# Performance work log

Measured on AMD Instinct MI355X. Metric: run time of the kernel, lower is better.

The kernel has to match this reference:

```python
import jax, jax.numpy as jnp
import numpy as np

NUM_HEADS = 16
PREFIX_LEN = 256


def setup_inputs() -> dict:
    key = jax.random.key(0)
    k1, k2, k3, k4 = jax.random.split(key, 4)
    bs, seq_len, dim = 2, 2048, 1024
    x = jax.random.normal(k1, (bs, seq_len, dim), dtype=jnp.float32)
    # torch Linear weights: (out_features, in_features)
    qkv_w = jax.random.normal(k2, (3 * dim, dim), dtype=jnp.float32) * (dim ** -0.5)
    proj_w = jax.random.normal(k3, (dim, dim), dtype=jnp.float32) * (dim ** -0.5)
    proj_b = jax.random.normal(k4, (dim,), dtype=jnp.float32) * 0.01
    # prefix tokens (visible to everyone): first PREFIX_LEN positions
    prefix_mask = (jnp.arange(seq_len)[None, :] < PREFIX_LEN) & jnp.ones((bs, 1), bool)
    return {"x": x, "qkv_w": qkv_w, "proj_w": proj_w, "proj_b": proj_b,
            "prefix_mask": prefix_mask, "num_patches": 2048}


def reference(x, qkv_w, proj_w, proj_b, prefix_mask, num_patches):
    bs, seq_len, dim = x.shape
    h, hd = NUM_HEADS, dim // NUM_HEADS

    # fused QKV projection (no bias)
    qkv = x @ qkv_w.T                                  # (bs, S, 3*dim)
    q, k, v = jnp.split(qkv, 3, axis=-1)
    q = q.reshape(bs, seq_len, h, hd).transpose(0, 2, 1, 3)  # (bs, h, S, hd)
    k = k.reshape(bs, seq_len, h, hd).transpose(0, 2, 1, 3)
    v = v.reshape(bs, seq_len, h, hd).transpose(0, 2, 1, 3)

    # prefix-causal mask: causal tril OR prefix columns, sliced to (S, S)
    tril = jnp.tril(jnp.ones((num_patches, num_patches), dtype=bool))[:seq_len, :seq_len]
    mask = jnp.logical_or(tril[None, :, :], prefix_mask[:, None, :])  # (bs, S, S)

    scores = jnp.einsum('bhqd,bhkd->bhqk', q, k) / jnp.sqrt(jnp.float32(hd))
    scores = jnp.where(mask[:, None, :, :], scores, -jnp.inf)
    attn = jax.nn.softmax(scores, axis=-1)
    out = jnp.einsum('bhqk,bhkd->bhqd', attn, v)       # (bs, h, S, hd)
    out = out.transpose(0, 2, 1, 3).reshape(bs, seq_len, dim)
    return out @ proj_w.T + proj_b
```

## Files before the change

kernel.cpp:

```cpp
#include <hip/hip_runtime.h>
#include <cstdint>

typedef __attribute__((ext_vector_type(8))) _Float16 half8;
typedef __attribute__((ext_vector_type(4))) _Float16 half4;
typedef __attribute__((ext_vector_type(2))) __fp16 fp16x2;
typedef __attribute__((ext_vector_type(4))) float f32x4;

union H8 { half8 v; unsigned u[4]; };
union H2U { fp16x2 h; unsigned u; };

__device__ __forceinline__ void gld_lds16(const void* g, void* l) {
  __builtin_amdgcn_global_load_lds(
      (const __attribute__((address_space(1))) unsigned int*)g,
      (__attribute__((address_space(3))) unsigned int*)l, 16, 0, 0);
}

__global__ __launch_bounds__(256) void cast3_kernel(
    const float* __restrict__ x, const float* __restrict__ w1,
    const float* __restrict__ w2, _Float16* __restrict__ out) {
  int i = blockIdx.x * 256 + threadIdx.x;
  const float* src;
  int off;
  if (i < 1048576)      { src = x;  off = i; }
  else if (i < 1835008) { src = w1; off = i - 1048576; }
  else                  { src = w2; off = i - 1835008; }
  float4 v = ((const float4*)src)[off];
  half4 h;
  h[0] = (_Float16)v.x; h[1] = (_Float16)v.y;
  h[2] = (_Float16)v.z; h[3] = (_Float16)v.w;
  ((half4*)out)[i] = h;
}

template <int EPI>
__global__ __launch_bounds__(256) void gemm_bt(
    const _Float16* __restrict__ A, const _Float16* __restrict__ B, int K,
    _Float16* __restrict__ Qb, _Float16* __restrict__ Kb, _Float16* __restrict__ VbT,
    float* __restrict__ Out, const float* __restrict__ Bias) {
  __shared__ _Float16 Asm[128 * 64];
  __shared__ _Float16 Bsm[128 * 64];
  const int tid = threadIdx.x;
  const int wave = tid >> 6, lane = tid & 63;
  const int l16 = lane & 15, lg = lane >> 4;
  const int m0 = blockIdx.y * 128, n0 = blockIdx.x * 128;
  const int wr = wave >> 1, wc = wave & 1;
  f32x4 acc[4][4] = {};

  int srow[4], sofs[4];
#pragma unroll
  for (int i = 0; i < 4; i++) {
    int c = tid + i * 256;
    srow[i] = c >> 3;
    sofs[i] = ((c & 7) ^ (srow[i] & 7)) * 8;
  }
  const int rb0 = ((lg) ^ (l16 & 7)) * 16;
  const int rb1 = ((4 + lg) ^ (l16 & 7)) * 16;

  for (int k0 = 0; k0 < K; k0 += 64) {
    __syncthreads();
#pragma unroll
    for (int i = 0; i < 4; i++) {
      int c = tid + i * 256;
      gld_lds16(A + (size_t)(m0 + srow[i]) * K + k0 + sofs[i], (char*)Asm + c * 16);
      gld_lds16(B + (size_t)(n0 + srow[i]) * K + k0 + sofs[i], (char*)Bsm + c * 16);
    }
    __syncthreads();
#pragma unroll
    for (int kc = 0; kc < 2; kc++) {
      const int rb = kc ? rb1 : rb0;
      half8 af[4], bf[4];
#pragma unroll
      for (int f = 0; f < 4; f++) {
        af[f] = *(const half8*)((char*)Asm + (wr * 64 + f * 16 + l16) * 128 + rb);
        bf[f] = *(const half8*)((char*)Bsm + (wc * 64 + f * 16 + l16) * 128 + rb);
      }
#pragma unroll
      for (int i = 0; i < 4; i++)
#pragma unroll
        for (int j = 0; j < 4; j++)
          acc[i][j] = __builtin_amdgcn_mfma_f32_16x16x32_f16(af[i], bf[j], acc[i][j], 0, 0, 0);
    }
  }

  if (EPI == 0) {
#pragma unroll
    for (int i = 0; i < 4; i++) {
      int mbase = m0 + wr * 64 + i * 16 + lg * 4;
      int b = mbase >> 11, s = mbase & 2047;
#pragma unroll
      for (int j = 0; j < 4; j++) {
        int n = n0 + wc * 64 + j * 16 + l16;
        int part = n >> 10, f = n & 1023;
        int h = f >> 6, d = f & 63;
        if (part == 2) {
          int x = s & 31;
          int sp = (s & ~31) | (((x >> 2) & 3) << 3) | (((x >> 4) & 1) << 2);
          half4 v;
          v[0] = (_Float16)acc[i][j][0]; v[1] = (_Float16)acc[i][j][1];
          v[2] = (_Float16)acc[i][j][2]; v[3] = (_Float16)acc[i][j][3];
          *(half4*)(VbT + (((size_t)b * 16 + h) * 64 + d) * 2048 + sp) = v;
        } else {
          _Float16* dst = (part == 0) ? Qb : Kb;
          float scale = (part == 0) ? 0.125f : 1.0f;
#pragma unroll
          for (int r = 0; r < 4; r++)
            dst[(((size_t)b * 16 + h) * 2048 + (s + r)) * 64 + d] =
                (_Float16)(acc[i][j][r] * scale);
        }
      }
    }
  } else {
#pragma unroll
    for (int i = 0; i < 4; i++) {
      int mbase = m0 + wr * 64 + i * 16 + lg * 4;
#pragma unroll
      for (int j = 0; j < 4; j++) {
        int n = n0 + wc * 64 + j * 16 + l16;
        float bias = Bias[n];
#pragma unroll
        for (int r = 0; r < 4; r++) {
          int m = mbase + r;
          Out[(size_t)m * 1024 + n] = acc[i][j][r] + bias;
        }
      }
    }
  }
}

__global__ __launch_bounds__(256) void attn_kernel(
    const _Float16* __restrict__ Qb, const _Float16* __restrict__ Kb,
    const _Float16* __restrict__ VbT, _Float16* __restrict__ AO) {
  __shared__ _Float16 Ks[2][64 * 64];
  __shared__ _Float16 Vt[2][64 * 64];
  const int bh = blockIdx.x;
  const int q0 = (31 - blockIdx.y) * 64;
  const int tid = threadIdx.x, wave = tid >> 6, lane = tid & 63;
  const int l16 = lane & 15, lg = lane >> 4;
  const int qw = q0 + wave * 16;
  const size_t bhbase = (size_t)bh * 2048 * 64;
  const _Float16* Kbb = Kb + bhbase;
  const _Float16* Vbb = VbT + bhbase;

  const int c0 = tid, c1 = tid + 256;
  const int kofs0 = ((c0 >> 3) * 64) + (((c0 & 7) ^ ((c0 >> 3) & 7)) * 8);
  const int kofs1 = ((c1 >> 3) * 64) + (((c1 & 7) ^ ((c1 >> 3) & 7)) * 8);
  const int vofs0 = ((c0 >> 3) * 2048) + (((c0 & 7) ^ ((c0 >> 3) & 7)) * 8);
  const int vofs1 = ((c1 >> 3) * 2048) + (((c1 & 7) ^ ((c1 >> 3) & 7)) * 8);

  half8 qf[2];
#pragma unroll
  for (int kc = 0; kc < 2; kc++)
    qf[kc] = *(const half8*)(Qb + bhbase + (size_t)(qw + l16) * 64 + kc * 32 + lg * 8);

  f32x4 oacc[4] = {};
  float mrun = -1e30f, lrun = 0.f;
  const int kend = (q0 + 64 > 256) ? (q0 + 64) : 256;

  const int xv = (l16 & 7) << 4;
  const int rb0 = l16 * 128 + ((lg * 16) ^ xv);
  const int rb1 = l16 * 128 + ((64 + lg * 16) ^ xv);

  auto STAGE = [&](int buf, int j0) {
    gld_lds16(Kbb + j0 * 64 + kofs0, (char*)Ks[buf] + c0 * 16);
    gld_lds16(Kbb + j0 * 64 + kofs1, (char*)Ks[buf] + c1 * 16);
    gld_lds16(Vbb + j0 + vofs0, (char*)Vt[buf] + c0 * 16);
    gld_lds16(Vbb + j0 + vofs1, (char*)Vt[buf] + c1 * 16);
  };

  STAGE(0, 0);
  int cur = 0;
  for (int j0 = 0; j0 < kend; j0 += 64) {
    __syncthreads();
    if (j0 + 64 < kend) STAGE(cur ^ 1, j0 + 64);
    const char* Kc = (const char*)Ks[cur];
    const char* Vc = (const char*)Vt[cur];

    f32x4 sf[4] = {};
#pragma unroll
    for (int kc = 0; kc < 2; kc++) {
      const int rb = kc ? rb1 : rb0;
#pragma unroll
      for (int jb = 0; jb < 4; jb++) {
        half8 kf = *(const half8*)(Kc + jb * 2048 + rb);
        sf[jb] = __builtin_amdgcn_mfma_f32_16x16x32_f16(kf, qf[kc], sf[jb], 0, 0, 0);
      }
    }

    if (j0 + 63 >= 256 && j0 + 63 > qw) {
      const int stok = qw + l16;
#pragma unroll
      for (int jb = 0; jb < 4; jb++)
#pragma unroll
        for (int r = 0; r < 4; r++) {
          int j = j0 + jb * 16 + lg * 4 + r;
          if (j > stok && j >= 256) sf[jb][r] = -1e30f;
        }
    }

    float a0 = fmaxf(fmaxf(sf[0][0], sf[0][1]), fmaxf(sf[0][2], sf[0][3]));
    float a1 = fmaxf(fmaxf(sf[1][0], sf[1][1]), fmaxf(sf[1][2], sf[1][3]));
    float a2 = fmaxf(fmaxf(sf[2][0], sf[2][1]), fmaxf(sf[2][2], sf[2][3]));
    float a3 = fmaxf(fmaxf(sf[3][0], sf[3][1]), fmaxf(sf[3][2], sf[3][3]));
    float mt = fmaxf(fmaxf(a0, a1), fmaxf(a2, a3));
    mt = fmaxf(mt, __shfl_xor(mt, 16));
    mt = fmaxf(mt, __shfl_xor(mt, 32));

    if (!__all(mt <= mrun + 5.545177f)) {
      float mn = fmaxf(mrun, mt);
      float corr = exp2f((mrun - mn) * 1.44269504f);
      mrun = mn;
      lrun *= corr;
#pragma unroll
      for (int db = 0; db < 4; db++) {
        oacc[db][0] *= corr; oacc[db][1] *= corr;
        oacc[db][2] *= corr; oacc[db][3] *= corr;
      }
    }
    const float nb = mrun * 1.44269504f;

    float p[16];
#pragma unroll
    for (int jb = 0; jb < 4; jb++)
#pragma unroll
      for (int r = 0; r < 4; r++)
        p[jb * 4 + r] = exp2f(sf[jb][r] * 1.44269504f - nb);

    float s0 = (p[0] + p[1]) + (p[2] + p[3]);
    float s1 = (p[4] + p[5]) + (p[6] + p[7]);
    float s2 = (p[8] + p[9]) + (p[10] + p[11]);
    float s3 = (p[12] + p[13]) + (p[14] + p[15]);
    float rs = (s0 + s1) + (s2 + s3);
    rs += __shfl_xor(rs, 16);
    rs += __shfl_xor(rs, 32);
    lrun += rs;

    H8 pf[2];
#pragma unroll
    for (int kc = 0; kc < 2; kc++) {
      H2U t0, t1, t2, t3;
      t0.h = __builtin_amdgcn_cvt_pkrtz(p[kc * 8 + 0], p[kc * 8 + 1]);
      t1.h = __builtin_amdgcn_cvt_pkrtz(p[kc * 8 + 2], p[kc * 8 + 3]);
      t2.h = __builtin_amdgcn_cvt_pkrtz(p[kc * 8 + 4], p[kc * 8 + 5]);
      t3.h = __builtin_amdgcn_cvt_pkrtz(p[kc * 8 + 6], p[kc * 8 + 7]);
      pf[kc].u[0] = t0.u; pf[kc].u[1] = t1.u;
      pf[kc].u[2] = t2.u; pf[kc].u[3] = t3.u;
    }

#pragma unroll
    for (int kc = 0; kc < 2; kc++) {
      const int rb = kc ? rb1 : rb0;
#pragma unroll
      for (int db = 0; db < 4; db++) {
        half8 vf = *(const half8*)(Vc + db * 2048 + rb);
        oacc[db] = __builtin_amdgcn_mfma_f32_16x16x32_f16(vf, pf[kc].v, oacc[db], 0, 0, 0);
      }
    }
    cur ^= 1;
  }

  const int b = bh >> 4, h = bh & 15;
  float inv = 1.0f / lrun;
  int q = qw + l16;
#pragma unroll
  for (int db = 0; db < 4; db++) {
    half4 o;
    o[0] = (_Float16)(oacc[db][0] * inv);
    o[1] = (_Float16)(oacc[db][1] * inv);
    o[2] = (_Float16)(oacc[db][2] * inv);
    o[3] = (_Float16)(oacc[db][3] * inv);
    *(half4*)(AO + ((size_t)b * 2048 + q) * 1024 + h * 64 + db * 16 + lg * 4) = o;
  }
}

extern "C" void kernel_launch(void* const* d_in, const int* in_sizes, int n_in,
                              void* d_out, int out_size, void* d_ws, size_t ws_size,
                              hipStream_t stream) {
  const float* x      = (const float*)d_in[0];
  const float* qkv_w  = (const float*)d_in[1];
  const float* proj_w = (const float*)d_in[2];
  const float* proj_b = (const float*)d_in[3];
  float* out = (float*)d_out;

  char* ws = (char*)d_ws;
  _Float16* Xh  = (_Float16*)(ws);
  _Float16* Wq  = (_Float16*)(ws + ((size_t)8 << 20));
  _Float16* Wp  = (_Float16*)(ws + ((size_t)14 << 20));
  _Float16* Qb  = (_Float16*)(ws + ((size_t)16 << 20));
  _Float16* Kb  = (_Float16*)(ws + ((size_t)24 << 20));
  _Float16* VbT = (_Float16*)(ws + ((size_t)32 << 20));
  _Float16* AO  = (_Float16*)(ws + ((size_t)40 << 20));

  cast3_kernel<<<8192, 256, 0, stream>>>(x, qkv_w, proj_w, Xh);

  gemm_bt<0><<<dim3(24, 32), 256, 0, stream>>>(Xh, Wq, 1024, Qb, Kb, VbT, nullptr, nullptr);
  attn_kernel<<<dim3(32, 32), 256, 0, stream>>>(Qb, Kb, VbT, AO);
  gemm_bt<1><<<dim3(8, 32), 256, 0, stream>>>(AO, Wp, 1024, nullptr, nullptr, nullptr, out, proj_b);
}
```

Measured before the change: 187.7 us.

## Load K/V fragments directly from global memory and remap attention grid for L2 locality

The attention kernel drops its LDS double-buffered staging of K and V tiles and the block-wide barriers, and each wave now loads its MFMA fragments straight from global memory. The launch becomes a flat 1D grid whose index mapping groups blocks of the same batch-head onto nearby XCD slots, so K/V reuse can be served from cache instead of shared memory. The softmax probabilities also reuse the score registers to ease register pressure. The risk is that each of the four waves re-reads the same K/V tiles from global/L2, with less coalesced 16-byte reads and no prefetch overlap.

```diff
diff --git a/kernel.cpp b/kernel.cpp
--- a/kernel.cpp
+++ b/kernel.cpp
@@ -129,60 +129,38 @@
 __global__ __launch_bounds__(256) void attn_kernel(
     const _Float16* __restrict__ Qb, const _Float16* __restrict__ Kb,
     const _Float16* __restrict__ VbT, _Float16* __restrict__ AO) {
-  __shared__ _Float16 Ks[2][64 * 64];
-  __shared__ _Float16 Vt[2][64 * 64];
-  const int bh = blockIdx.x;
-  const int q0 = (31 - blockIdx.y) * 64;
+  const int flat = blockIdx.x;
+  const int bh = (flat & 7) * 4 + (flat >> 8);
+  const int qt = (flat >> 3) & 31;
+  const int q0 = (31 - qt) * 64;
   const int tid = threadIdx.x, wave = tid >> 6, lane = tid & 63;
   const int l16 = lane & 15, lg = lane >> 4;
   const int qw = q0 + wave * 16;
   const size_t bhbase = (size_t)bh * 2048 * 64;
-  const _Float16* Kbb = Kb + bhbase;
-  const _Float16* Vbb = VbT + bhbase;
-
-  const int c0 = tid, c1 = tid + 256;
-  const int kofs0 = ((c0 >> 3) * 64) + (((c0 & 7) ^ ((c0 >> 3) & 7)) * 8);
-  const int kofs1 = ((c1 >> 3) * 64) + (((c1 & 7) ^ ((c1 >> 3) & 7)) * 8);
-  const int vofs0 = ((c0 >> 3) * 2048) + (((c0 & 7) ^ ((c0 >> 3) & 7)) * 8);
-  const int vofs1 = ((c1 >> 3) * 2048) + (((c1 & 7) ^ ((c1 >> 3) & 7)) * 8);
 
   half8 qf[2];
 #pragma unroll
   for (int kc = 0; kc < 2; kc++)
     qf[kc] = *(const half8*)(Qb + bhbase + (size_t)(qw + l16) * 64 + kc * 32 + lg * 8);
+
+  const _Float16* Kt = Kb + bhbase + l16 * 64 + lg * 8;
+  const _Float16* Vt = VbT + bhbase + l16 * 2048 + lg * 8;
 
   f32x4 oacc[4] = {};
   float mrun = -1e30f, lrun = 0.f;
   const int kend = (q0 + 64 > 256) ? (q0 + 64) : 256;
 
-  const int xv = (l16 & 7) << 4;
-  const int rb0 = l16 * 128 + ((lg * 16) ^ xv);
-  const int rb1 = l16 * 128 + ((64 + lg * 16) ^ xv);
-
-  auto STAGE = [&](int buf, int j0) {
-    gld_lds16(Kbb + j0 * 64 + kofs0, (char*)Ks[buf] + c0 * 16);
-    gld_lds16(Kbb + j0 * 64 + kofs1, (char*)Ks[buf] + c1 * 16);
-    gld_lds16(Vbb + j0 + vofs0, (char*)Vt[buf] + c0 * 16);
-    gld_lds16(Vbb + j0 + vofs1, (char*)Vt[buf] + c1 * 16);
-  };
-
-  STAGE(0, 0);
-  int cur = 0;
-  for (int j0 = 0; j0 < kend; j0 += 64) {
-    __syncthreads();
-    if (j0 + 64 < kend) STAGE(cur ^ 1, j0 + 64);
-    const char* Kc = (const char*)Ks[cur];
-    const char* Vc = (const char*)Vt[cur];
-
+  for (int j0 = 0; j0 < kend; j0 += 64, Kt += 64 * 64, Vt += 64) {
     f32x4 sf[4] = {};
 #pragma unroll
     for (int kc = 0; kc < 2; kc++) {
-      const int rb = kc ? rb1 : rb0;
-#pragma unroll
-      for (int jb = 0; jb < 4; jb++) {
-        half8 kf = *(const half8*)(Kc + jb * 2048 + rb);
-        sf[jb] = __builtin_amdgcn_mfma_f32_16x16x32_f16(kf, qf[kc], sf[jb], 0, 0, 0);
-      }
+      half8 kf[4];
+#pragma unroll
+      for (int jb = 0; jb < 4; jb++)
+        kf[jb] = *(const half8*)(Kt + jb * 1024 + kc * 32);
+#pragma unroll
+      for (int jb = 0; jb < 4; jb++)
+        sf[jb] = __builtin_amdgcn_mfma_f32_16x16x32_f16(kf[jb], qf[kc], sf[jb], 0, 0, 0);
     }
 
     if (j0 + 63 >= 256 && j0 + 63 > qw) {
@@ -217,17 +195,16 @@
     }
     const float nb = mrun * 1.44269504f;
 
-    float p[16];
 #pragma unroll
     for (int jb = 0; jb < 4; jb++)
 #pragma unroll
       for (int r = 0; r < 4; r++)
-        p[jb * 4 + r] = exp2f(sf[jb][r] * 1.44269504f - nb);
-
-    float s0 = (p[0] + p[1]) + (p[2] + p[3]);
-    float s1 = (p[4] + p[5]) + (p[6] + p[7]);
-    float s2 = (p[8] + p[9]) + (p[10] + p[11]);
-    float s3 = (p[12] + p[13]) + (p[14] + p[15]);
+        sf[jb][r] = exp2f(sf[jb][r] * 1.44269504f - nb);
+
+    float s0 = (sf[0][0] + sf[0][1]) + (sf[0][2] + sf[0][3]);
+    float s1 = (sf[1][0] + sf[1][1]) + (sf[1][2] + sf[1][3]);
+    float s2 = (sf[2][0] + sf[2][1]) + (sf[2][2] + sf[2][3]);
+    float s3 = (sf[3][0] + sf[3][1]) + (sf[3][2] + sf[3][3]);
     float rs = (s0 + s1) + (s2 + s3);
     rs += __shfl_xor(rs, 16);
     rs += __shfl_xor(rs, 32);
@@ -237,24 +214,24 @@
 #pragma unroll
     for (int kc = 0; kc < 2; kc++) {
       H2U t0, t1, t2, t3;
-      t0.h = __builtin_amdgcn_cvt_pkrtz(p[kc * 8 + 0], p[kc * 8 + 1]);
-      t1.h = __builtin_amdgcn_cvt_pkrtz(p[kc * 8 + 2], p[kc * 8 + 3]);
-      t2.h = __builtin_amdgcn_cvt_pkrtz(p[kc * 8 + 4], p[kc * 8 + 5]);
-      t3.h = __builtin_amdgcn_cvt_pkrtz(p[kc * 8 + 6], p[kc * 8 + 7]);
+      t0.h = __builtin_amdgcn_cvt_pkrtz(sf[kc * 2][0], sf[kc * 2][1]);
+      t1.h = __builtin_amdgcn_cvt_pkrtz(sf[kc * 2][2], sf[kc * 2][3]);
+      t2.h = __builtin_amdgcn_cvt_pkrtz(sf[kc * 2 + 1][0], sf[kc * 2 + 1][1]);
+      t3.h = __builtin_amdgcn_cvt_pkrtz(sf[kc * 2 + 1][2], sf[kc * 2 + 1][3]);
       pf[kc].u[0] = t0.u; pf[kc].u[1] = t1.u;
       pf[kc].u[2] = t2.u; pf[kc].u[3] = t3.u;
     }
 
 #pragma unroll
     for (int kc = 0; kc < 2; kc++) {
-      const int rb = kc ? rb1 : rb0;
-#pragma unroll
-      for (int db = 0; db < 4; db++) {
-        half8 vf = *(const half8*)(Vc + db * 2048 + rb);
-        oacc[db] = __builtin_amdgcn_mfma_f32_16x16x32_f16(vf, pf[kc].v, oacc[db], 0, 0, 0);
-      }
-    }
-    cur ^= 1;
+      half8 vf[4];
+#pragma unroll
+      for (int db = 0; db < 4; db++)
+        vf[db] = *(const half8*)(Vt + db * 16 * 2048 + kc * 32);
+#pragma unroll
+      for (int db = 0; db < 4; db++)
+        oacc[db] = __builtin_amdgcn_mfma_f32_16x16x32_f16(vf[db], pf[kc].v, oacc[db], 0, 0, 0);
+    }
   }
 
   const int b = bh >> 4, h = bh & 15;
@@ -292,6 +269,6 @@
   cast3_kernel<<<8192, 256, 0, stream>>>(x, qkv_w, proj_w, Xh);
 
   gemm_bt<0><<<dim3(24, 32), 256, 0, stream>>>(Xh, Wq, 1024, Qb, Kb, VbT, nullptr, nullptr);
-  attn_kernel<<<dim3(32, 32), 256, 0, stream>>>(Qb, Kb, VbT, AO);
+  attn_kernel<<<1024, 256, 0, stream>>>(Qb, Kb, VbT, AO);
   gemm_bt<1><<<dim3(8, 32), 256, 0, stream>>>(AO, Wp, 1024, nullptr, nullptr, nullptr, out, proj_b);
 }
```

Measured after the change: 368.8 us. 96.5% more time.
